# Optimization experiments

Measured on AMD Instinct MI355X. Metric: run time of the kernel, lower is better.

The kernel has to match this reference:

```python
import jax, jax.numpy as jnp
import numpy as np

N_NODES = 100000
IN_F = 128
OUT_F = 64
N_EDGES = 1600000


def setup_inputs() -> dict:
    key = jax.random.key(0)
    k1, k2, k3, k4 = jax.random.split(key, 4)
    x = jax.random.normal(k1, (N_NODES, IN_F), dtype=jnp.float32)
    edge_index = jax.random.randint(k2, (2, N_EDGES), 0, N_NODES, dtype=jnp.int64)
    # GCNConv learned params (glorot-ish scale)
    W = jax.random.normal(k3, (IN_F, OUT_F), dtype=jnp.float32) * (1.0 / np.sqrt(IN_F))
    b = jnp.zeros((OUT_F,), dtype=jnp.float32)
    return {"x": x, "edge_index": edge_index, "W": W, "b": b}


def reference(x, edge_index, W, b):
    # PyG GCNConv with defaults: add self-loops, symmetric degree normalization.
    n = x.shape[0]
    self_loops = jnp.arange(n, dtype=edge_index.dtype)
    row = jnp.concatenate([edge_index[0], self_loops])  # source nodes
    col = jnp.concatenate([edge_index[1], self_loops])  # target nodes

    # in-degree (incl. self-loops) at target nodes, edge_weight = 1
    deg = jax.ops.segment_sum(jnp.ones_like(col, dtype=x.dtype), col, num_segments=n)
    deg_inv_sqrt = jnp.where(deg > 0, jax.lax.rsqrt(deg), 0.0)
    norm = deg_inv_sqrt[row] * deg_inv_sqrt[col]  # [E+N]

    h = x @ W  # [N, out]
    msgs = norm[:, None] * h[row]  # gather + scale, [E+N, out]
    out = jax.ops.segment_sum(msgs, col, num_segments=n)  # scatter-add
    return out + b
```

## Files before the change

kernel.cpp:

```cpp
#include <hip/hip_runtime.h>
#include <hip/hip_bf16.h>

constexpr int N_NODES = 100000;
constexpr int IN_F    = 128;
constexpr int OUT_F   = 64;
constexpr int N_EDGES = 1600000;

constexpr int NPB     = 128;
constexpr int NB      = (N_NODES + NPB - 1) / NPB;
constexpr int B_HIST  = 512;
constexpr int EPB     = N_EDGES / B_HIST;
constexpr int STAGE_CAP = 2816;

typedef short bf16x8 __attribute__((ext_vector_type(8)));
typedef float f32x4  __attribute__((ext_vector_type(4)));

static __device__ __forceinline__ unsigned short f2b(float f) {
    __hip_bfloat16 h = __float2bfloat16(f);
    return *reinterpret_cast<unsigned short*>(&h);
}
static __device__ __forceinline__ float blo(unsigned int u) {
    return __uint_as_float(u << 16);
}
static __device__ __forceinline__ float bhi(unsigned int u) {
    return __uint_as_float(u & 0xffff0000u);
}

__global__ __launch_bounds__(256) void hist_kernel(const int* __restrict__ col,
                                                   int* __restrict__ hist_g) {
    __shared__ int hist[NB];
    for (int i = threadIdx.x; i < NB; i += 256) hist[i] = 0;
    __syncthreads();
    const int beg = blockIdx.x * EPB, end = beg + EPB;
    for (int e = beg + threadIdx.x; e < end; e += 256)
        atomicAdd(&hist[col[e] >> 7], 1);
    __syncthreads();
    for (int i = threadIdx.x; i < NB; i += 256)
        hist_g[i * B_HIST + blockIdx.x] = hist[i];
}

__global__ __launch_bounds__(512) void scanbins_kernel(int* __restrict__ hist_g,
                                                       int* __restrict__ binTotal) {
    __shared__ int s[B_HIST];
    const int bin = blockIdx.x, t = threadIdx.x;
    int v = hist_g[bin * B_HIST + t];
    s[t] = v;
    __syncthreads();
#pragma unroll
    for (int off = 1; off < B_HIST; off <<= 1) {
        int u = (t >= off) ? s[t - off] : 0;
        __syncthreads();
        s[t] += u;
        __syncthreads();
    }
    hist_g[bin * B_HIST + t] = s[t] - v;
    if (t == B_HIST - 1) binTotal[bin] = s[t];
}

__global__ __launch_bounds__(1024) void scanoff_kernel(const int* __restrict__ binTotal,
                                                       int* __restrict__ binStart,
                                                       int* __restrict__ offsets) {
    __shared__ int s[1024];
    const int t = threadIdx.x;
    int v = (t < NB) ? binTotal[t] : 0;
    s[t] = v;
    __syncthreads();
#pragma unroll
    for (int off = 1; off < 1024; off <<= 1) {
        int u = (t >= off) ? s[t - off] : 0;
        __syncthreads();
        s[t] += u;
        __syncthreads();
    }
    if (t < NB) binStart[t] = s[t] - v;
    if (t == 0) {
        binStart[NB] = N_EDGES;
        offsets[N_NODES] = N_EDGES;
    }
}

__global__ __launch_bounds__(256) void scatter_kernel(const int* __restrict__ eidx,
                                                      const int* __restrict__ hist_g,
                                                      const int* __restrict__ binStart,
                                                      uint2* __restrict__ pairs) {
    __shared__ int cur[NB];
    for (int i = threadIdx.x; i < NB; i += 256)
        cur[i] = binStart[i] + hist_g[i * B_HIST + blockIdx.x];
    __syncthreads();
    const int beg = blockIdx.x * EPB, end = beg + EPB;
    for (int e = beg + threadIdx.x; e < end; e += 256) {
        int row = eidx[e];
        int col = eidx[N_EDGES + e];
        int p = atomicAdd(&cur[col >> 7], 1);
        pairs[p] = make_uint2((unsigned)col, (unsigned)row);
    }
}

__global__ __launch_bounds__(256) void finalize_kernel(const uint2* __restrict__ pairs,
                                                       const int* __restrict__ binStart,
                                                       int* __restrict__ offsets,
                                                       float* __restrict__ dis,
                                                       int* __restrict__ sorted_row) {
    __shared__ uint2 st[STAGE_CAP];
    __shared__ int cnt[NPB], s[NPB], curs[NPB];
    const int b = blockIdx.x, t = threadIdx.x;
    const int beg = binStart[b], end = binStart[b + 1];
    const int n0 = b << 7;
    const int nn = min(NPB, N_NODES - n0);
    const int size = end - beg;

    for (int i = t; i < NPB; i += 256) cnt[i] = 0;
    __syncthreads();
    for (int i = t; i < size; i += 256) {
        uint2 p = pairs[beg + i];
        if (i < STAGE_CAP) st[i] = p;
        atomicAdd(&cnt[p.x & (NPB - 1)], 1);
    }
    __syncthreads();
    if (t < NPB) s[t] = cnt[t];
    __syncthreads();
#pragma unroll
    for (int off = 1; off < NPB; off <<= 1) {
        int u = (t < NPB && t >= off) ? s[t - off] : 0;
        __syncthreads();
        if (t < NPB) s[t] += u;
        __syncthreads();
    }
    if (t < NPB) {
        int ex = s[t] - cnt[t];
        curs[t] = ex;
        if (t < nn) {
            offsets[n0 + t] = beg + ex;
            dis[n0 + t] = rsqrtf((float)cnt[t] + 1.0f);
        }
    }
    __syncthreads();
    for (int i = t; i < size; i += 256) {
        uint2 p = (i < STAGE_CAP) ? st[i] : pairs[beg + i];
        int q = atomicAdd(&curs[p.x & (NPB - 1)], 1);
        sorted_row[beg + q] = (int)p.y;
    }
}

__global__ __launch_bounds__(256) void wt_kernel(const float* __restrict__ W,
                                                 unsigned short* __restrict__ WT) {
    int idx = blockIdx.x * 256 + threadIdx.x;
    if (idx < IN_F * OUT_F) {
        int k = idx >> 6, n = idx & 63;
        WT[n * IN_F + k] = f2b(W[idx]);
    }
}

constexpr int GEMM_ROWS = 64;
__global__ __launch_bounds__(256) void gemm_kernel(const float* __restrict__ x,
                                                   const unsigned short* __restrict__ WT,
                                                   unsigned short* __restrict__ h) {
    __shared__ unsigned short Xs[GEMM_ROWS][IN_F];
    __shared__ unsigned short Ws[OUT_F][IN_F];
    const int tid = threadIdx.x;
    const int row0 = blockIdx.x * GEMM_ROWS;

#pragma unroll
    for (int j = 0; j < 4; ++j) {
        int g  = tid + j * 256;
        int n  = g >> 4;
        int k8 = (g & 15) * 8;
        bf16x8 v = *(const bf16x8*)&WT[n * IN_F + k8];
        *(bf16x8*)&Ws[n][k8 ^ ((n & 7) << 3)] = v;
    }
    {
        int r    = tid >> 2;
        int grow = row0 + r;
        if (grow >= N_NODES) grow = N_NODES - 1;
        int ks   = (tid & 3) * 32;
        const float4* xp = (const float4*)x + (long)grow * (IN_F / 4) + (ks >> 2);
        int sw = (r & 7) << 3;
#pragma unroll
        for (int j = 0; j < 8; ++j) {
            float4 xv = xp[j];
            unsigned int u0 = (unsigned int)f2b(xv.x) | ((unsigned int)f2b(xv.y) << 16);
            unsigned int u1 = (unsigned int)f2b(xv.z) | ((unsigned int)f2b(xv.w) << 16);
            uint2 p; p.x = u0; p.y = u1;
            *(uint2*)&Xs[r][(ks + j * 4) ^ sw] = p;
        }
    }
    __syncthreads();

    const int w    = tid >> 6;
    const int lane = tid & 63;
    const int ml   = lane & 15;
    const int kg   = lane >> 4;

    const int rowA = w * 16 + ml;
    const int swA  = (rowA & 7) << 3;

    bf16x8 a[4];
#pragma unroll
    for (int kt = 0; kt < 4; ++kt)
        a[kt] = *(const bf16x8*)&Xs[rowA][(kt * 32 + kg * 8) ^ swA];

    f32x4 acc[4];
#pragma unroll
    for (int ct = 0; ct < 4; ++ct) acc[ct] = (f32x4)(0.0f);

#pragma unroll
    for (int ct = 0; ct < 4; ++ct) {
        int n  = ct * 16 + ml;
        int sw = (n & 7) << 3;
#pragma unroll
        for (int kt = 0; kt < 4; ++kt) {
            bf16x8 bv = *(const bf16x8*)&Ws[n][(kt * 32 + kg * 8) ^ sw];
            acc[ct] = __builtin_amdgcn_mfma_f32_16x16x32_bf16(a[kt], bv, acc[ct], 0, 0, 0);
        }
    }

    const int grow0 = row0 + w * 16 + kg * 4;
#pragma unroll
    for (int ct = 0; ct < 4; ++ct) {
#pragma unroll
        for (int i = 0; i < 4; ++i) {
            int r = grow0 + i;
            if (r < N_NODES)
                h[(long)r * OUT_F + ct * 16 + ml] = f2b(acc[ct][i]);
        }
    }
}

__global__ __launch_bounds__(256) void gather_kernel(const int* __restrict__ sorted_row,
                                                     const int* __restrict__ offsets,
                                                     const float* __restrict__ dis,
                                                     const unsigned int* __restrict__ h2,
                                                     const float* __restrict__ b,
                                                     float* __restrict__ out) {
    int gtid = blockIdx.x * blockDim.x + threadIdx.x;
    int node = gtid >> 6;
    if (node >= N_NODES) return;
    int lane = threadIdx.x & 63;
    int half = lane >> 5;
    int sl   = lane & 31;

    int beg = offsets[node];
    int end = offsets[node + 1];
    float dc = dis[node];

    float ax = 0.0f, ay = 0.0f;
    for (int i = beg + half; i < end; i += 2) {
        int row  = sorted_row[i];
        float wn = dis[row] * dc;
        unsigned int u = h2[row * 32 + sl];
        ax += wn * blo(u);
        ay += wn * bhi(u);
    }
    ax += __shfl_xor(ax, 32);
    ay += __shfl_xor(ay, 32);

    if (half == 0) {
        unsigned int us = h2[node * 32 + sl];
        float sc = dc * dc;
        float2 bv = ((const float2*)b)[sl];
        float2 o;
        o.x = ax + bv.x + sc * blo(us);
        o.y = ay + bv.y + sc * bhi(us);
        ((float2*)out)[node * 32 + sl] = o;
    }
}

extern "C" void kernel_launch(void* const* d_in, const int* in_sizes, int n_in,
                              void* d_out, int out_size, void* d_ws, size_t ws_size,
                              hipStream_t stream) {
    const float* x   = (const float*)d_in[0];
    const int*   idx = (const int*)d_in[1];
    const float* W   = (const float*)d_in[2];
    const float* b   = (const float*)d_in[3];
    float*       out = (float*)d_out;

    int* p          = (int*)d_ws;
    uint2* pairs    = (uint2*)p;            p += 2 * N_EDGES;
    int* hist_g     = p;                    p += NB * B_HIST;
    int* binTotal   = p;                    p += 784;
    int* binStart   = p;                    p += 784;
    int* offsets    = p;                    p += N_NODES + 4;
    float* dis      = (float*)p;            p += N_NODES;
    int* sorted_row = p;                    p += N_EDGES;
    unsigned short* WT = (unsigned short*)p; p += IN_F * OUT_F / 2;
    unsigned short* hb = (unsigned short*)p;

    hist_kernel<<<B_HIST, 256, 0, stream>>>(idx + N_EDGES, hist_g);
    scanbins_kernel<<<NB, 512, 0, stream>>>(hist_g, binTotal);
    scanoff_kernel<<<1, 1024, 0, stream>>>(binTotal, binStart, offsets);
    scatter_kernel<<<B_HIST, 256, 0, stream>>>(idx, hist_g, binStart, pairs);
    wt_kernel<<<(IN_F * OUT_F + 255) / 256, 256, 0, stream>>>(W, WT);
    gemm_kernel<<<(N_NODES + GEMM_ROWS - 1) / GEMM_ROWS, 256, 0, stream>>>(x, WT, hb);
    finalize_kernel<<<NB, 256, 0, stream>>>(pairs, binStart, offsets, dis, sorted_row);
    gather_kernel<<<(N_NODES * 64 + 255) / 256, 256, 0, stream>>>(
        sorted_row, offsets, dis, (const unsigned int*)hb, b, out);
}
```

Before: 247.4 us.

## Replace per-node sort with 64-node bins and shared-memory atomic aggregation

```diff
diff --git a/kernel.cpp b/kernel.cpp
--- a/kernel.cpp
+++ b/kernel.cpp
@@ -6,11 +6,10 @@
 constexpr int OUT_F   = 64;
 constexpr int N_EDGES = 1600000;
 
-constexpr int NPB     = 128;
-constexpr int NB      = (N_NODES + NPB - 1) / NPB;
-constexpr int B_HIST  = 512;
-constexpr int EPB     = N_EDGES / B_HIST;
-constexpr int STAGE_CAP = 2816;
+constexpr int NPB    = 64;
+constexpr int NB     = (N_NODES + NPB - 1) / NPB;
+constexpr int B_SORT = 256;
+constexpr int EPB    = N_EDGES / B_SORT;
 
 typedef short bf16x8 __attribute__((ext_vector_type(8)));
 typedef float f32x4  __attribute__((ext_vector_type(4)));
@@ -31,39 +30,40 @@
     __shared__ int hist[NB];
     for (int i = threadIdx.x; i < NB; i += 256) hist[i] = 0;
     __syncthreads();
-    const int beg = blockIdx.x * EPB, end = beg + EPB;
-    for (int e = beg + threadIdx.x; e < end; e += 256)
-        atomicAdd(&hist[col[e] >> 7], 1);
+    const int beg = blockIdx.x * EPB;
+    for (int e = beg + threadIdx.x; e < beg + EPB; e += 256)
+        atomicAdd(&hist[col[e] >> 6], 1);
     __syncthreads();
     for (int i = threadIdx.x; i < NB; i += 256)
-        hist_g[i * B_HIST + blockIdx.x] = hist[i];
-}
-
-__global__ __launch_bounds__(512) void scanbins_kernel(int* __restrict__ hist_g,
+        hist_g[i * B_SORT + blockIdx.x] = hist[i];
+}
+
+__global__ __launch_bounds__(256) void scanbins_kernel(int* __restrict__ hist_g,
                                                        int* __restrict__ binTotal) {
-    __shared__ int s[B_HIST];
+    __shared__ int s[B_SORT];
     const int bin = blockIdx.x, t = threadIdx.x;
-    int v = hist_g[bin * B_HIST + t];
+    int v = hist_g[bin * B_SORT + t];
     s[t] = v;
     __syncthreads();
 #pragma unroll
-    for (int off = 1; off < B_HIST; off <<= 1) {
+    for (int off = 1; off < B_SORT; off <<= 1) {
         int u = (t >= off) ? s[t - off] : 0;
         __syncthreads();
         s[t] += u;
         __syncthreads();
     }
-    hist_g[bin * B_HIST + t] = s[t] - v;
-    if (t == B_HIST - 1) binTotal[bin] = s[t];
+    hist_g[bin * B_SORT + t] = s[t] - v;
+    if (t == B_SORT - 1) binTotal[bin] = s[t];
 }
 
 __global__ __launch_bounds__(1024) void scanoff_kernel(const int* __restrict__ binTotal,
-                                                       int* __restrict__ binStart,
-                                                       int* __restrict__ offsets) {
+                                                       int* __restrict__ binStart) {
     __shared__ int s[1024];
     const int t = threadIdx.x;
-    int v = (t < NB) ? binTotal[t] : 0;
-    s[t] = v;
+    const int i0 = 2 * t, i1 = 2 * t + 1;
+    int v0 = (i0 < NB) ? binTotal[i0] : 0;
+    int v1 = (i1 < NB) ? binTotal[i1] : 0;
+    s[t] = v0 + v1;
     __syncthreads();
 #pragma unroll
     for (int off = 1; off < 1024; off <<= 1) {
@@ -72,74 +72,43 @@
         s[t] += u;
         __syncthreads();
     }
-    if (t < NB) binStart[t] = s[t] - v;
-    if (t == 0) {
-        binStart[NB] = N_EDGES;
-        offsets[N_NODES] = N_EDGES;
-    }
+    int base = s[t] - v0 - v1;
+    if (i0 < NB) binStart[i0] = base;
+    if (i1 < NB) binStart[i1] = base + v0;
+    if (t == 0) binStart[NB] = N_EDGES;
 }
 
 __global__ __launch_bounds__(256) void scatter_kernel(const int* __restrict__ eidx,
                                                       const int* __restrict__ hist_g,
                                                       const int* __restrict__ binStart,
-                                                      uint2* __restrict__ pairs) {
+                                                      unsigned int* __restrict__ packs) {
     __shared__ int cur[NB];
     for (int i = threadIdx.x; i < NB; i += 256)
-        cur[i] = binStart[i] + hist_g[i * B_HIST + blockIdx.x];
-    __syncthreads();
-    const int beg = blockIdx.x * EPB, end = beg + EPB;
-    for (int e = beg + threadIdx.x; e < end; e += 256) {
+        cur[i] = binStart[i] + hist_g[i * B_SORT + blockIdx.x];
+    __syncthreads();
+    const int beg = blockIdx.x * EPB;
+    for (int e = beg + threadIdx.x; e < beg + EPB; e += 256) {
         int row = eidx[e];
         int col = eidx[N_EDGES + e];
-        int p = atomicAdd(&cur[col >> 7], 1);
-        pairs[p] = make_uint2((unsigned)col, (unsigned)row);
-    }
-}
-
-__global__ __launch_bounds__(256) void finalize_kernel(const uint2* __restrict__ pairs,
-                                                       const int* __restrict__ binStart,
-                                                       int* __restrict__ offsets,
-                                                       float* __restrict__ dis,
-                                                       int* __restrict__ sorted_row) {
-    __shared__ uint2 st[STAGE_CAP];
-    __shared__ int cnt[NPB], s[NPB], curs[NPB];
+        int p = atomicAdd(&cur[col >> 6], 1);
+        packs[p] = ((unsigned)row << 6) | (unsigned)(col & 63);
+    }
+}
+
+__global__ __launch_bounds__(256) void degdis_kernel(const unsigned int* __restrict__ packs,
+                                                     const int* __restrict__ binStart,
+                                                     float* __restrict__ dis) {
+    __shared__ int cnt[NPB];
     const int b = blockIdx.x, t = threadIdx.x;
+    if (t < NPB) cnt[t] = 0;
+    __syncthreads();
     const int beg = binStart[b], end = binStart[b + 1];
-    const int n0 = b << 7;
-    const int nn = min(NPB, N_NODES - n0);
-    const int size = end - beg;
-
-    for (int i = t; i < NPB; i += 256) cnt[i] = 0;
-    __syncthreads();
-    for (int i = t; i < size; i += 256) {
-        uint2 p = pairs[beg + i];
-        if (i < STAGE_CAP) st[i] = p;
-        atomicAdd(&cnt[p.x & (NPB - 1)], 1);
-    }
-    __syncthreads();
-    if (t < NPB) s[t] = cnt[t];
-    __syncthreads();
-#pragma unroll
-    for (int off = 1; off < NPB; off <<= 1) {
-        int u = (t < NPB && t >= off) ? s[t - off] : 0;
-        __syncthreads();
-        if (t < NPB) s[t] += u;
-        __syncthreads();
-    }
-    if (t < NPB) {
-        int ex = s[t] - cnt[t];
-        curs[t] = ex;
-        if (t < nn) {
-            offsets[n0 + t] = beg + ex;
-            dis[n0 + t] = rsqrtf((float)cnt[t] + 1.0f);
-        }
-    }
-    __syncthreads();
-    for (int i = t; i < size; i += 256) {
-        uint2 p = (i < STAGE_CAP) ? st[i] : pairs[beg + i];
-        int q = atomicAdd(&curs[p.x & (NPB - 1)], 1);
-        sorted_row[beg + q] = (int)p.y;
-    }
+    for (int i = beg + t; i < end; i += 256)
+        atomicAdd(&cnt[packs[i] & 63], 1);
+    __syncthreads();
+    const int n0 = b << 6;
+    if (t < NPB && n0 + t < N_NODES)
+        dis[n0 + t] = rsqrtf((float)cnt[t] + 1.0f);
 }
 
 __global__ __launch_bounds__(256) void wt_kernel(const float* __restrict__ W,
@@ -180,8 +149,8 @@
             float4 xv = xp[j];
             unsigned int u0 = (unsigned int)f2b(xv.x) | ((unsigned int)f2b(xv.y) << 16);
             unsigned int u1 = (unsigned int)f2b(xv.z) | ((unsigned int)f2b(xv.w) << 16);
-            uint2 p; p.x = u0; p.y = u1;
-            *(uint2*)&Xs[r][(ks + j * 4) ^ sw] = p;
+            uint2 pr; pr.x = u0; pr.y = u1;
+            *(uint2*)&Xs[r][(ks + j * 4) ^ sw] = pr;
         }
     }
     __syncthreads();
@@ -226,42 +195,45 @@
     }
 }
 
-__global__ __launch_bounds__(256) void gather_kernel(const int* __restrict__ sorted_row,
-                                                     const int* __restrict__ offsets,
+__global__ __launch_bounds__(256) void gather_kernel(const unsigned int* __restrict__ packs,
+                                                     const int* __restrict__ binStart,
                                                      const float* __restrict__ dis,
                                                      const unsigned int* __restrict__ h2,
-                                                     const float* __restrict__ b,
+                                                     const float* __restrict__ bias,
                                                      float* __restrict__ out) {
-    int gtid = blockIdx.x * blockDim.x + threadIdx.x;
-    int node = gtid >> 6;
-    if (node >= N_NODES) return;
-    int lane = threadIdx.x & 63;
-    int half = lane >> 5;
-    int sl   = lane & 31;
-
-    int beg = offsets[node];
-    int end = offsets[node + 1];
-    float dc = dis[node];
-
-    float ax = 0.0f, ay = 0.0f;
-    for (int i = beg + half; i < end; i += 2) {
-        int row  = sorted_row[i];
-        float wn = dis[row] * dc;
+    __shared__ float acc[NPB][OUT_F + 1];
+    __shared__ float disL[NPB];
+    const int b = blockIdx.x, t = threadIdx.x;
+    const int n0 = b << 6;
+
+    for (int i = t; i < NPB * (OUT_F + 1); i += 256) ((float*)acc)[i] = 0.0f;
+    if (t < NPB) disL[t] = (n0 + t < N_NODES) ? dis[n0 + t] : 0.0f;
+    __syncthreads();
+
+    const int lane   = t & 63;
+    const int sl     = lane & 31;
+    const int stream = ((t >> 6) << 1) | (lane >> 5);
+    const int beg = binStart[b], end = binStart[b + 1];
+
+    for (int i = beg + stream; i < end; i += 8) {
+        unsigned int pk = packs[i];
+        int row = pk >> 6;
+        int c   = pk & 63;
+        float wn = dis[row] * disL[c];
         unsigned int u = h2[row * 32 + sl];
-        ax += wn * blo(u);
-        ay += wn * bhi(u);
-    }
-    ax += __shfl_xor(ax, 32);
-    ay += __shfl_xor(ay, 32);
-
-    if (half == 0) {
-        unsigned int us = h2[node * 32 + sl];
-        float sc = dc * dc;
-        float2 bv = ((const float2*)b)[sl];
-        float2 o;
-        o.x = ax + bv.x + sc * blo(us);
-        o.y = ay + bv.y + sc * bhi(us);
-        ((float2*)out)[node * 32 + sl] = o;
+        atomicAdd(&acc[c][2 * sl], wn * blo(u));
+        atomicAdd(&acc[c][2 * sl + 1], wn * bhi(u));
+    }
+    __syncthreads();
+
+    const int w = t >> 6;
+    for (int c = w; c < NPB; c += 4) {
+        int node = n0 + c;
+        if (node >= N_NODES) break;
+        unsigned int us = h2[node * 32 + (lane >> 1)];
+        float selfv = (lane & 1) ? bhi(us) : blo(us);
+        float dcc = disL[c];
+        out[node * 64 + lane] = acc[c][lane] + bias[lane] + dcc * dcc * selfv;
     }
 }
 
@@ -274,24 +246,23 @@
     const float* b   = (const float*)d_in[3];
     float*       out = (float*)d_out;
 
-    int* p          = (int*)d_ws;
-    uint2* pairs    = (uint2*)p;            p += 2 * N_EDGES;
-    int* hist_g     = p;                    p += NB * B_HIST;
-    int* binTotal   = p;                    p += 784;
-    int* binStart   = p;                    p += 784;
-    int* offsets    = p;                    p += N_NODES + 4;
-    float* dis      = (float*)p;            p += N_NODES;
-    int* sorted_row = p;                    p += N_EDGES;
+    int* p = (int*)d_ws;
+    unsigned int* packs = (unsigned int*)p;  p += N_EDGES;
+    int* hist_g   = p;                       p += NB * B_SORT;
+    int* binTotal = p;                       p += NB + 4;
+    int* binStart = p;                       p += NB + 4;
+    float* dis    = (float*)p;               p += N_NODES;
+    p = (int*)(((uintptr_t)p + 15) & ~(uintptr_t)15);
     unsigned short* WT = (unsigned short*)p; p += IN_F * OUT_F / 2;
     unsigned short* hb = (unsigned short*)p;
 
-    hist_kernel<<<B_HIST, 256, 0, stream>>>(idx + N_EDGES, hist_g);
-    scanbins_kernel<<<NB, 512, 0, stream>>>(hist_g, binTotal);
-    scanoff_kernel<<<1, 1024, 0, stream>>>(binTotal, binStart, offsets);
-    scatter_kernel<<<B_HIST, 256, 0, stream>>>(idx, hist_g, binStart, pairs);
+    hist_kernel<<<B_SORT, 256, 0, stream>>>(idx + N_EDGES, hist_g);
+    scanbins_kernel<<<NB, B_SORT, 0, stream>>>(hist_g, binTotal);
+    scanoff_kernel<<<1, 1024, 0, stream>>>(binTotal, binStart);
+    scatter_kernel<<<B_SORT, 256, 0, stream>>>(idx, hist_g, binStart, packs);
     wt_kernel<<<(IN_F * OUT_F + 255) / 256, 256, 0, stream>>>(W, WT);
     gemm_kernel<<<(N_NODES + GEMM_ROWS - 1) / GEMM_ROWS, 256, 0, stream>>>(x, WT, hb);
-    finalize_kernel<<<NB, 256, 0, stream>>>(pairs, binStart, offsets, dis, sorted_row);
-    gather_kernel<<<(N_NODES * 64 + 255) / 256, 256, 0, stream>>>(
-        sorted_row, offsets, dis, (const unsigned int*)hb, b, out);
-}
+    degdis_kernel<<<NB, 256, 0, stream>>>(packs, binStart, dis);
+    gather_kernel<<<NB, 256, 0, stream>>>(packs, binStart, dis,
+                                          (const unsigned int*)hb, b, out);
+}
```

Measured after the change: 750.0 us. +203.2%, slower.
